# Kernel tuning notes

Measured on AMD Instinct MI355X. Metric: run time of the kernel, lower is better.

Reference implementation:

```python
import jax, jax.numpy as jnp
import numpy as np

B, N, H, A, S = 8, 8192, 256, 64, 32  # batch, nodes, hidden, annotation, sub_graphs


def _mysoftmax(x):
    # exp, zero out where x <= 0, normalize over last dim, nan (0/0) -> 0
    x_exp = jnp.where(x > 0, jnp.exp(x), 0.0)
    part = jnp.sum(x_exp, axis=-1, keepdims=True)
    # safe divide: where partition == 0 the faithful result after nan_to_num is 0
    return jnp.where(part > 0, x_exp / jnp.where(part > 0, part, 1.0), 0.0)


def setup_inputs() -> dict:
    key = jax.random.key(0)
    k1, k2, k3, k4, k5, k6 = jax.random.split(key, 6)
    x = jax.random.normal(k1, (B, N, H + A), dtype=jnp.float32)
    node_map = jax.random.uniform(k2, (B, S, N), dtype=jnp.float32)
    lim = 1.0 / np.sqrt(H + A)
    Wi = jax.random.uniform(k3, (H, H + A), minval=-lim, maxval=lim, dtype=jnp.float32)
    bi = jax.random.uniform(k4, (H,), minval=-lim, maxval=lim, dtype=jnp.float32)
    Wj = jax.random.uniform(k5, (H, H + A), minval=-lim, maxval=lim, dtype=jnp.float32)
    bj = jax.random.uniform(k6, (H,), minval=-lim, maxval=lim, dtype=jnp.float32)
    return {"x": x, "node_map": node_map, "Wi": Wi, "bi": bi, "Wj": Wj, "bj": bj}


def reference(x, node_map, Wi, bi, Wj, bj):
    # gated node features: sigmoid(fc_i(x)) * tanh(fc_j(x))  -> [B, N, H]
    x_sigm = jax.nn.sigmoid(jnp.einsum('bnf,hf->bnh', x, Wi) + bi)
    x_tanh = jnp.tanh(jnp.einsum('bnf,hf->bnh', x, Wj) + bj)
    x_all = x_sigm * x_tanh
    # per-node L2 norm -> [B, 1, N]
    x_norm = jnp.linalg.norm(x_all, axis=-1)[:, None, :]
    # scaled subgraph map and masked softmax over nodes -> [B, S, N]
    weight = _mysoftmax(node_map * x_norm)
    # weighted sum over nodes (replaces [B,S,N,H] broadcast) -> [B, S, H]
    pooled = jnp.einsum('bsn,bnh->bsh', weight, x_all)
    return jnp.tanh(pooled), weight[..., None]
```

## Files before the change

### kernel.cpp

```cpp
#include <hip/hip_runtime.h>
#include <cstdint>
#include <cstddef>

typedef unsigned short u16;
typedef unsigned int   u32;
using short8 = __attribute__((ext_vector_type(8))) short;
using f32x4  = __attribute__((ext_vector_type(4))) float;

#define NB    8
#define NN    8192
#define HH    256
#define FF    320
#define SS    32
#define NROWS 65536
#define NCH   64

__device__ __forceinline__ u16 f2bf(float f) {
    union { float f; u32 u; } v; v.f = f;
    u32 r = v.u + 0x7fffu + ((v.u >> 16) & 1u);
    return (u16)(r >> 16);
}
__device__ __forceinline__ u32 pk2h(float lo, float hi) {
    union { float f; u32 u; } a, b; a.f = lo; b.f = hi;
    return __builtin_amdgcn_perm(b.u + 0x8000u, a.u + 0x8000u, 0x07060302u);
}
__device__ __forceinline__ short8 pack8(float4 a, float4 b) {
    union { u32 u[4]; short8 s; } r;
    r.u[0] = pk2h(a.x, a.y); r.u[1] = pk2h(a.z, a.w);
    r.u[2] = pk2h(b.x, b.y); r.u[3] = pk2h(b.z, b.w);
    return r.s;
}

__global__ __launch_bounds__(256) void prep_w(const float* __restrict__ Wi,
                                              const float* __restrict__ Wj,
                                              u16* __restrict__ Wb) {
    int idx = blockIdx.x * 256 + threadIdx.x;
    float v = (idx < 81920) ? Wi[idx] : Wj[idx - 81920];
    Wb[idx] = f2bf(v);
}

__global__ __launch_bounds__(256) void cast_x(const float* __restrict__ x,
                                              u16* __restrict__ xb) {
    int t = blockIdx.x * 256 + threadIdx.x;
    #pragma unroll
    for (int i = 0; i < 4; ++i) {
        size_t g = (size_t)i * 655360 + t;
        float4 a = *reinterpret_cast<const float4*>(x + g * 8);
        float4 b = *reinterpret_cast<const float4*>(x + g * 8 + 4);
        *reinterpret_cast<short8*>(xb + g * 8) = pack8(a, b);
    }
}

__global__ __launch_bounds__(512, 4) void gemm_gate_pre(
    const u16* __restrict__ xbg, const u16* __restrict__ Wb,
    const float* __restrict__ bi, const float* __restrict__ bj,
    u16* __restrict__ xa, float* __restrict__ normsq_p)
{
    __shared__ u16 lB[5 * 8192];

    const int bx   = blockIdx.x;
    const int xcd  = bx & 7;
    const int ht   = (bx >> 3) & 3;
    const int slot = bx >> 5;
    const int mb   = xcd + slot * 8;
    const int m0   = mb * 256;
    const int h0   = ht * 64;
    const int b_idx = m0 >> 13;
    const int n0    = m0 & 8191;

    const int tid  = threadIdx.x;
    const int w    = tid >> 6;
    const int lane = tid & 63;
    const int quad = lane >> 4;
    const int l15  = lane & 15;

    {
        const int rsub = lane >> 3;
        const int kg   = (lane & 7) ^ rsub;
        #pragma unroll
        for (int kt = 0; kt < 5; ++kt) {
            #pragma unroll
            for (int j = 0; j < 2; ++j) {
                int sl  = w * 2 + j;
                int row = sl * 8 + rsub;
                int mat = row >> 6, hl = row & 63;
                const u16* gsrc = Wb + mat * 81920 + (size_t)(h0 + hl) * FF + kt * 64 + kg * 8;
                u16* ldst = &lB[kt * 8192 + sl * 512];
                __builtin_amdgcn_global_load_lds(
                    (const __attribute__((address_space(1))) void*)gsrc,
                    (__attribute__((address_space(3))) void*)ldst, 16, 0, 0);
            }
        }
    }

    const u16* xr0 = xbg + (size_t)(m0 + w * 32 + l15) * FF + quad * 8;
    const u16* xr1 = xr0 + 16 * FF;

    f32x4 acc[8][2];
    #pragma unroll
    for (int a = 0; a < 8; ++a)
        #pragma unroll
        for (int m = 0; m < 2; ++m) acc[a][m] = (f32x4){0.f, 0.f, 0.f, 0.f};

    short8 af[4][2];
    #pragma unroll
    for (int s = 0; s < 3; ++s) {
        af[s][0] = *reinterpret_cast<const short8*>(xr0 + s * 32);
        af[s][1] = *reinterpret_cast<const short8*>(xr1 + s * 32);
    }

    __syncthreads();

    #pragma unroll
    for (int ks = 0; ks < 10; ++ks) {
        const int kt  = ks >> 1, kk = ks & 1;
        const int cur = ks & 3;
        if (ks < 7) {
            const int nx = (ks + 3) & 3;
            af[nx][0] = *reinterpret_cast<const short8*>(xr0 + (ks + 3) * 32);
            af[nx][1] = *reinterpret_cast<const short8*>(xr1 + (ks + 3) * 32);
        }
        #pragma unroll
        for (int mn = 0; mn < 8; ++mn) {
            int c = mn * 16 + l15;
            short8 bv = *reinterpret_cast<const short8*>(
                &lB[kt * 8192 + c * 64 + (((kk * 4 + quad) ^ (c & 7)) << 3)]);
            acc[mn][0] = __builtin_amdgcn_mfma_f32_16x16x32_bf16(af[cur][0], bv, acc[mn][0], 0, 0, 0);
            acc[mn][1] = __builtin_amdgcn_mfma_f32_16x16x32_bf16(af[cur][1], bv, acc[mn][1], 0, 0, 0);
        }
    }

    float s0[2][4];
    #pragma unroll
    for (int mt = 0; mt < 2; ++mt)
        #pragma unroll
        for (int r = 0; r < 4; ++r) s0[mt][r] = 0.f;

    #pragma unroll
    for (int hq = 0; hq < 4; ++hq) {
        int h = h0 + hq * 16 + l15;
        float bi_v = bi[h], bj_v = bj[h];
        #pragma unroll
        for (int mt = 0; mt < 2; ++mt) {
            float xall[4];
            #pragma unroll
            for (int r = 0; r < 4; ++r) {
                float yi = acc[hq][mt][r] + bi_v;
                float yj = acc[hq + 4][mt][r] + bj_v;
                float sg = 1.f / (1.f + __expf(-yi));
                float e2 = __expf(-2.f * yj);
                float th = (1.f - e2) / (1.f + e2);
                float xv = sg * th;
                xall[r] = xv;
                s0[mt][r] += xv * xv;
            }
            uint2 pk;
            pk.x = pk2h(xall[0], xall[1]);
            pk.y = pk2h(xall[2], xall[3]);
            size_t o = (size_t)b_idx * ((size_t)HH * NN) + (size_t)h * NN
                     + (size_t)(n0 + w * 32 + mt * 16 + quad * 4);
            *reinterpret_cast<uint2*>(&xa[o]) = pk;
        }
    }
    #pragma unroll
    for (int m = 1; m <= 8; m <<= 1) {
        #pragma unroll
        for (int mt = 0; mt < 2; ++mt)
            #pragma unroll
            for (int r = 0; r < 4; ++r)
                s0[mt][r] += __shfl_xor(s0[mt][r], m, 64);
    }
    if (l15 == 0) {
        #pragma unroll
        for (int mt = 0; mt < 2; ++mt)
            #pragma unroll
            for (int r = 0; r < 4; ++r)
                normsq_p[ht * NROWS + m0 + w * 32 + mt * 16 + quad * 4 + r] = s0[mt][r];
    }
}

__global__ __launch_bounds__(512, 4) void gemm_gate_f32(
    const float* __restrict__ x, const u16* __restrict__ Wb,
    const float* __restrict__ bi, const float* __restrict__ bj,
    u16* __restrict__ xa, float* __restrict__ normsq_p)
{
    __shared__ u16 lB[5 * 8192];

    const int bx   = blockIdx.x;
    const int xcd  = bx & 7;
    const int ht   = (bx >> 3) & 3;
    const int slot = bx >> 5;
    const int mb   = xcd + slot * 8;
    const int m0   = mb * 256;
    const int h0   = ht * 64;
    const int b_idx = m0 >> 13;
    const int n0    = m0 & 8191;

    const int tid  = threadIdx.x;
    const int w    = tid >> 6;
    const int lane = tid & 63;
    const int quad = lane >> 4;
    const int l15  = lane & 15;

    {
        const int rsub = lane >> 3;
        const int kg   = (lane & 7) ^ rsub;
        #pragma unroll
        for (int kt = 0; kt < 5; ++kt) {
            #pragma unroll
            for (int j = 0; j < 2; ++j) {
                int sl  = w * 2 + j;
                int row = sl * 8 + rsub;
                int mat = row >> 6, hl = row & 63;
                const u16* gsrc = Wb + mat * 81920 + (size_t)(h0 + hl) * FF + kt * 64 + kg * 8;
                u16* ldst = &lB[kt * 8192 + sl * 512];
                __builtin_amdgcn_global_load_lds(
                    (const __attribute__((address_space(1))) void*)gsrc,
                    (__attribute__((address_space(3))) void*)ldst, 16, 0, 0);
            }
        }
    }

    const float* xb = x + (size_t)(m0 + w * 32 + l15) * FF + quad * 8;

    f32x4 acc[8][2];
    #pragma unroll
    for (int a = 0; a < 8; ++a)
        #pragma unroll
        for (int m = 0; m < 2; ++m) acc[a][m] = (f32x4){0.f, 0.f, 0.f, 0.f};

    float4 pre[3][2][2];
    #pragma unroll
    for (int s = 0; s < 2; ++s)
        #pragma unroll
        for (int mt = 0; mt < 2; ++mt) {
            pre[s][mt][0] = *reinterpret_cast<const float4*>(xb + mt * 16 * FF + s * 32);
            pre[s][mt][1] = *reinterpret_cast<const float4*>(xb + mt * 16 * FF + s * 32 + 4);
        }

    __syncthreads();

    #pragma unroll
    for (int ks = 0; ks < 10; ++ks) {
        const int kt  = ks >> 1, kk = ks & 1;
        const int cur = ks % 3;
        if (ks < 8) {
            const int nx = (ks + 2) % 3;
            const int f  = (ks + 2) * 32;
            #pragma unroll
            for (int mt = 0; mt < 2; ++mt) {
                pre[nx][mt][0] = *reinterpret_cast<const float4*>(xb + mt * 16 * FF + f);
                pre[nx][mt][1] = *reinterpret_cast<const float4*>(xb + mt * 16 * FF + f + 4);
            }
        }
        short8 af0 = pack8(pre[cur][0][0], pre[cur][0][1]);
        short8 af1 = pack8(pre[cur][1][0], pre[cur][1][1]);
        #pragma unroll
        for (int mn = 0; mn < 8; ++mn) {
            int c = mn * 16 + l15;
            short8 bv = *reinterpret_cast<const short8*>(
                &lB[kt * 8192 + c * 64 + (((kk * 4 + quad) ^ (c & 7)) << 3)]);
            acc[mn][0] = __builtin_amdgcn_mfma_f32_16x16x32_bf16(af0, bv, acc[mn][0], 0, 0, 0);
            acc[mn][1] = __builtin_amdgcn_mfma_f32_16x16x32_bf16(af1, bv, acc[mn][1], 0, 0, 0);
        }
    }

    float s0[2][4];
    #pragma unroll
    for (int mt = 0; mt < 2; ++mt)
        #pragma unroll
        for (int r = 0; r < 4; ++r) s0[mt][r] = 0.f;

    #pragma unroll
    for (int hq = 0; hq < 4; ++hq) {
        int h = h0 + hq * 16 + l15;
        float bi_v = bi[h], bj_v = bj[h];
        #pragma unroll
        for (int mt = 0; mt < 2; ++mt) {
            float xall[4];
            #pragma unroll
            for (int r = 0; r < 4; ++r) {
                float yi = acc[hq][mt][r] + bi_v;
                float yj = acc[hq + 4][mt][r] + bj_v;
                float sg = 1.f / (1.f + __expf(-yi));
                float e2 = __expf(-2.f * yj);
                float th = (1.f - e2) / (1.f + e2);
                float xv = sg * th;
                xall[r] = xv;
                s0[mt][r] += xv * xv;
            }
            uint2 pk;
            pk.x = pk2h(xall[0], xall[1]);
            pk.y = pk2h(xall[2], xall[3]);
            size_t o = (size_t)b_idx * ((size_t)HH * NN) + (size_t)h * NN
                     + (size_t)(n0 + w * 32 + mt * 16 + quad * 4);
            *reinterpret_cast<uint2*>(&xa[o]) = pk;
        }
    }
    #pragma unroll
    for (int m = 1; m <= 8; m <<= 1) {
        #pragma unroll
        for (int mt = 0; mt < 2; ++mt)
            #pragma unroll
            for (int r = 0; r < 4; ++r)
                s0[mt][r] += __shfl_xor(s0[mt][r], m, 64);
    }
    if (l15 == 0) {
        #pragma unroll
        for (int mt = 0; mt < 2; ++mt)
            #pragma unroll
            for (int r = 0; r < 4; ++r)
                normsq_p[ht * NROWS + m0 + w * 32 + mt * 16 + quad * 4 + r] = s0[mt][r];
    }
}

__global__ __launch_bounds__(1024) void softmax_k(
    const float* __restrict__ nm, const float* __restrict__ normsq_p,
    float* __restrict__ out1)
{
    __shared__ float red[16];
    int bs = blockIdx.x;
    int b  = bs >> 5;
    const float* src = nm + (size_t)bs * NN;
    float* dst       = out1 + (size_t)bs * NN;
    const float* ns  = normsq_p + (size_t)b * NN;
    int tid = threadIdx.x;
    float e[8];
    float sum = 0.f;
    #pragma unroll
    for (int i = 0; i < 8; ++i) {
        int n = i * 1024 + tid;
        float nsq = ns[n] + ns[n + NROWS] + ns[n + 2 * NROWS] + ns[n + 3 * NROWS];
        float logit = src[n] * sqrtf(nsq);
        float v = (logit > 0.f) ? __expf(logit) : 0.f;
        e[i] = v;
        sum += v;
    }
    #pragma unroll
    for (int m = 1; m <= 32; m <<= 1) sum += __shfl_xor(sum, m, 64);
    int w = tid >> 6, lane = tid & 63;
    if (lane == 0) red[w] = sum;
    __syncthreads();
    float part = 0.f;
    #pragma unroll
    for (int j = 0; j < 16; ++j) part += red[j];
    float inv = (part > 0.f) ? (1.f / part) : 0.f;
    #pragma unroll
    for (int i = 0; i < 8; ++i) dst[i * 1024 + tid] = e[i] * inv;
}

__global__ __launch_bounds__(256) void pooled_k(
    const u16* __restrict__ xa, const float* __restrict__ wgt,
    float* __restrict__ part)
{
    __shared__ u16 lw[32 * 136];
    int bx = blockIdx.x;
    int b  = bx >> 6, c = bx & 63;
    int n0 = c * 128;
    int tid = threadIdx.x, w = tid >> 6, lane = tid & 63, quad = lane >> 4, l15 = lane & 15;

    const u16* ab = xa + (size_t)b * ((size_t)HH * NN) + n0;

    short8 av[2][4];
    #pragma unroll
    for (int htl = 0; htl < 4; ++htl) {
        int h = w * 64 + htl * 16 + l15;
        av[0][htl] = *reinterpret_cast<const short8*>(ab + (size_t)h * NN + quad * 8);
    }

    {
        int s  = tid >> 3;
        int jq = (tid & 7) * 16;
        const float* src = wgt + (size_t)(b * SS + s) * NN + n0 + jq;
        #pragma unroll
        for (int q = 0; q < 4; ++q) {
            float4 v = *reinterpret_cast<const float4*>(src + q * 4);
            uint2 pk;
            pk.x = pk2h(v.x, v.y);
            pk.y = pk2h(v.z, v.w);
            *reinterpret_cast<uint2*>(&lw[s * 136 + jq + q * 4]) = pk;
        }
    }
    __syncthreads();

    f32x4 acc[4][2];
    #pragma unroll
    for (int a = 0; a < 4; ++a)
        #pragma unroll
        for (int s = 0; s < 2; ++s) acc[a][s] = (f32x4){0.f, 0.f, 0.f, 0.f};

    #pragma unroll
    for (int ks = 0; ks < 4; ++ks) {
        const int cur = ks & 1, nxt = cur ^ 1;
        if (ks < 3) {
            #pragma unroll
            for (int htl = 0; htl < 4; ++htl) {
                int h = w * 64 + htl * 16 + l15;
                av[nxt][htl] = *reinterpret_cast<const short8*>(
                    ab + (size_t)h * NN + (ks + 1) * 32 + quad * 8);
            }
        }
        #pragma unroll
        for (int st = 0; st < 2; ++st) {
            int s = st * 16 + l15;
            short8 bv = *reinterpret_cast<const short8*>(&lw[s * 136 + ks * 32 + quad * 8]);
            #pragma unroll
            for (int htl = 0; htl < 4; ++htl)
                acc[htl][st] = __builtin_amdgcn_mfma_f32_16x16x32_bf16(av[cur][htl], bv, acc[htl][st], 0, 0, 0);
        }
    }
    float* pb = part + (size_t)(b * NCH + c) * 8192;
    #pragma unroll
    for (int htl = 0; htl < 4; ++htl) {
        #pragma unroll
        for (int st = 0; st < 2; ++st) {
            int h = w * 64 + htl * 16 + quad * 4;
            int s = st * 16 + l15;
            *reinterpret_cast<f32x4*>(&pb[s * 256 + h]) = acc[htl][st];
        }
    }
}

__global__ __launch_bounds__(256) void reduce_tanh(const float* __restrict__ part,
                                                   float* __restrict__ out0)
{
    int gid = blockIdx.x * 256 + threadIdx.x;
    int b = gid >> 13, r = gid & 8191;
    const float* p = part + (size_t)b * NCH * 8192 + r;
    float s = 0.f;
    #pragma unroll
    for (int c = 0; c < NCH; ++c) s += p[(size_t)c * 8192];
    out0[gid] = tanhf(s);
}

extern "C" void kernel_launch(void* const* d_in, const int* in_sizes, int n_in,
                              void* d_out, int out_size, void* d_ws, size_t ws_size,
                              hipStream_t stream) {
    const float* x  = (const float*)d_in[0];
    const float* nm = (const float*)d_in[1];
    const float* Wi = (const float*)d_in[2];
    const float* bi = (const float*)d_in[3];
    const float* Wj = (const float*)d_in[4];
    const float* bj = (const float*)d_in[5];
    float* out0 = (float*)d_out;
    float* out1 = out0 + NB * SS * HH;

    char* ws = (char*)d_ws;
    size_t off = 0;
    u16*   Wb       = (u16*)(ws + off);  off += 327680;
    u16*   xa       = (u16*)(ws + off);  off += 33554432;
    float* normsq_p = (float*)(ws + off); off += 1048576;
    float* part     = (float*)(ws + off); off += 16777216;
    u16*   xb       = (u16*)(ws + off);
    const size_t need_fast = off + 41943040;

    prep_w<<<640, 256, 0, stream>>>(Wi, Wj, Wb);
    if (ws_size >= need_fast) {
        cast_x       <<<2560, 256, 0, stream>>>(x, xb);
        gemm_gate_pre<<<1024, 512, 0, stream>>>(xb, Wb, bi, bj, xa, normsq_p);
    } else {
        gemm_gate_f32<<<1024, 512, 0, stream>>>(x, Wb, bi, bj, xa, normsq_p);
    }
    softmax_k  <<<256, 1024, 0, stream>>>(nm, normsq_p, out1);
    pooled_k   <<<512,  256, 0, stream>>>(xa, out1, part);
    reduce_tanh<<<256,  256, 0, stream>>>(part, out0);
}
```

Measured before the change: 215.0 us.

## Retile gate GEMM warps to 2x2, merge prep kernels, halve pooled chunks

The gate GEMM now splits its eight waves into a 4x2 grid, each covering 64 rows by 32 columns of both the i and j outputs. This replaces 32 rows by all 64 columns and is meant to raise A-fragment reuse and cut global A loads per wave. The norm partials grow from four to eight slices, so softmax now sums eight. The weight and x cast kernels are merged into one launch. Pooling uses 256-node chunks, halving the partial buffer and the reduction work, at the cost of fewer blocks and more accumulator registers per wave.

Result: no change. 211.7 us (-1.5%).

```diff
diff --git a/kernel.cpp b/kernel.cpp
--- a/kernel.cpp
+++ b/kernel.cpp
@@ -13,7 +13,7 @@
 #define FF    320
 #define SS    32
 #define NROWS 65536
-#define NCH   64
+#define NCH   32
 
 __device__ __forceinline__ u16 f2bf(float f) {
     union { float f; u32 u; } v; v.f = f;
@@ -31,23 +31,25 @@
     return r.s;
 }
 
-__global__ __launch_bounds__(256) void prep_w(const float* __restrict__ Wi,
-                                              const float* __restrict__ Wj,
-                                              u16* __restrict__ Wb) {
-    int idx = blockIdx.x * 256 + threadIdx.x;
-    float v = (idx < 81920) ? Wi[idx] : Wj[idx - 81920];
-    Wb[idx] = f2bf(v);
-}
-
-__global__ __launch_bounds__(256) void cast_x(const float* __restrict__ x,
-                                              u16* __restrict__ xb) {
-    int t = blockIdx.x * 256 + threadIdx.x;
-    #pragma unroll
-    for (int i = 0; i < 4; ++i) {
-        size_t g = (size_t)i * 655360 + t;
-        float4 a = *reinterpret_cast<const float4*>(x + g * 8);
-        float4 b = *reinterpret_cast<const float4*>(x + g * 8 + 4);
-        *reinterpret_cast<short8*>(xb + g * 8) = pack8(a, b);
+__global__ __launch_bounds__(256) void prep_all(const float* __restrict__ Wi,
+                                                const float* __restrict__ Wj,
+                                                const float* __restrict__ x,
+                                                u16* __restrict__ Wb,
+                                                u16* __restrict__ xb) {
+    int bx = blockIdx.x;
+    if (bx < 640) {
+        int idx = bx * 256 + threadIdx.x;
+        float v = (idx < 81920) ? Wi[idx] : Wj[idx - 81920];
+        Wb[idx] = f2bf(v);
+    } else {
+        int t = (bx - 640) * 256 + threadIdx.x;
+        #pragma unroll
+        for (int i = 0; i < 4; ++i) {
+            size_t g = (size_t)i * 655360 + t;
+            float4 a = *reinterpret_cast<const float4*>(x + g * 8);
+            float4 b = *reinterpret_cast<const float4*>(x + g * 8 + 4);
+            *reinterpret_cast<short8*>(xb + g * 8) = pack8(a, b);
+        }
     }
 }
 
@@ -73,6 +75,8 @@
     const int lane = tid & 63;
     const int quad = lane >> 4;
     const int l15  = lane & 15;
+    const int rg   = w >> 1;
+    const int cg   = w & 1;
 
     {
         const int rsub = lane >> 3;
@@ -93,60 +97,61 @@
         }
     }
 
-    const u16* xr0 = xbg + (size_t)(m0 + w * 32 + l15) * FF + quad * 8;
-    const u16* xr1 = xr0 + 16 * FF;
-
-    f32x4 acc[8][2];
-    #pragma unroll
-    for (int a = 0; a < 8; ++a)
-        #pragma unroll
-        for (int m = 0; m < 2; ++m) acc[a][m] = (f32x4){0.f, 0.f, 0.f, 0.f};
-
-    short8 af[4][2];
-    #pragma unroll
-    for (int s = 0; s < 3; ++s) {
-        af[s][0] = *reinterpret_cast<const short8*>(xr0 + s * 32);
-        af[s][1] = *reinterpret_cast<const short8*>(xr1 + s * 32);
-    }
+    const u16* xr = xbg + (size_t)(m0 + rg * 64 + l15) * FF + quad * 8;
+
+    f32x4 acc[4][4];
+    #pragma unroll
+    for (int a = 0; a < 4; ++a)
+        #pragma unroll
+        for (int m = 0; m < 4; ++m) acc[a][m] = (f32x4){0.f, 0.f, 0.f, 0.f};
+
+    short8 af[2][4];
+    #pragma unroll
+    for (int mt = 0; mt < 4; ++mt)
+        af[0][mt] = *reinterpret_cast<const short8*>(xr + mt * 16 * FF);
+
+    const int cb0 = cg * 32, cb1 = cg * 32 + 16, cb2 = 64 + cg * 32, cb3 = 64 + cg * 32 + 16;
 
     __syncthreads();
 
     #pragma unroll
     for (int ks = 0; ks < 10; ++ks) {
         const int kt  = ks >> 1, kk = ks & 1;
-        const int cur = ks & 3;
-        if (ks < 7) {
-            const int nx = (ks + 3) & 3;
-            af[nx][0] = *reinterpret_cast<const short8*>(xr0 + (ks + 3) * 32);
-            af[nx][1] = *reinterpret_cast<const short8*>(xr1 + (ks + 3) * 32);
-        }
-        #pragma unroll
-        for (int mn = 0; mn < 8; ++mn) {
-            int c = mn * 16 + l15;
+        const int cur = ks & 1, nxt = cur ^ 1;
+        if (ks < 9) {
+            #pragma unroll
+            for (int mt = 0; mt < 4; ++mt)
+                af[nxt][mt] = *reinterpret_cast<const short8*>(xr + mt * 16 * FF + (ks + 1) * 32);
+        }
+        const int cbs[4] = {cb0, cb1, cb2, cb3};
+        #pragma unroll
+        for (int mn = 0; mn < 4; ++mn) {
+            int c = cbs[mn] + l15;
             short8 bv = *reinterpret_cast<const short8*>(
                 &lB[kt * 8192 + c * 64 + (((kk * 4 + quad) ^ (c & 7)) << 3)]);
-            acc[mn][0] = __builtin_amdgcn_mfma_f32_16x16x32_bf16(af[cur][0], bv, acc[mn][0], 0, 0, 0);
-            acc[mn][1] = __builtin_amdgcn_mfma_f32_16x16x32_bf16(af[cur][1], bv, acc[mn][1], 0, 0, 0);
-        }
-    }
-
-    float s0[2][4];
-    #pragma unroll
-    for (int mt = 0; mt < 2; ++mt)
+            #pragma unroll
+            for (int mt = 0; mt < 4; ++mt)
+                acc[mn][mt] = __builtin_amdgcn_mfma_f32_16x16x32_bf16(af[cur][mt], bv, acc[mn][mt], 0, 0, 0);
+        }
+    }
+
+    float s0[4][4];
+    #pragma unroll
+    for (int mt = 0; mt < 4; ++mt)
         #pragma unroll
         for (int r = 0; r < 4; ++r) s0[mt][r] = 0.f;
 
     #pragma unroll
-    for (int hq = 0; hq < 4; ++hq) {
-        int h = h0 + hq * 16 + l15;
+    for (int hq = 0; hq < 2; ++hq) {
+        int h = h0 + cg * 32 + hq * 16 + l15;
         float bi_v = bi[h], bj_v = bj[h];
         #pragma unroll
-        for (int mt = 0; mt < 2; ++mt) {
+        for (int mt = 0; mt < 4; ++mt) {
             float xall[4];
             #pragma unroll
             for (int r = 0; r < 4; ++r) {
                 float yi = acc[hq][mt][r] + bi_v;
-                float yj = acc[hq + 4][mt][r] + bj_v;
+                float yj = acc[hq + 2][mt][r] + bj_v;
                 float sg = 1.f / (1.f + __expf(-yi));
                 float e2 = __expf(-2.f * yj);
                 float th = (1.f - e2) / (1.f + e2);
@@ -158,24 +163,24 @@
             pk.x = pk2h(xall[0], xall[1]);
             pk.y = pk2h(xall[2], xall[3]);
             size_t o = (size_t)b_idx * ((size_t)HH * NN) + (size_t)h * NN
-                     + (size_t)(n0 + w * 32 + mt * 16 + quad * 4);
+                     + (size_t)(n0 + rg * 64 + mt * 16 + quad * 4);
             *reinterpret_cast<uint2*>(&xa[o]) = pk;
         }
     }
     #pragma unroll
     for (int m = 1; m <= 8; m <<= 1) {
         #pragma unroll
-        for (int mt = 0; mt < 2; ++mt)
+        for (int mt = 0; mt < 4; ++mt)
             #pragma unroll
             for (int r = 0; r < 4; ++r)
                 s0[mt][r] += __shfl_xor(s0[mt][r], m, 64);
     }
     if (l15 == 0) {
         #pragma unroll
-        for (int mt = 0; mt < 2; ++mt)
+        for (int mt = 0; mt < 4; ++mt)
             #pragma unroll
             for (int r = 0; r < 4; ++r)
-                normsq_p[ht * NROWS + m0 + w * 32 + mt * 16 + quad * 4 + r] = s0[mt][r];
+                normsq_p[(ht * 2 + cg) * NROWS + m0 + rg * 64 + mt * 16 + quad * 4 + r] = s0[mt][r];
     }
 }
 
@@ -330,7 +335,9 @@
     #pragma unroll
     for (int i = 0; i < 8; ++i) {
         int n = i * 1024 + tid;
-        float nsq = ns[n] + ns[n + NROWS] + ns[n + 2 * NROWS] + ns[n + 3 * NROWS];
+        float nsq = 0.f;
+        #pragma unroll
+        for (int j = 0; j < 8; ++j) nsq += ns[n + j * NROWS];
         float logit = src[n] * sqrtf(nsq);
         float v = (logit > 0.f) ? __expf(logit) : 0.f;
         e[i] = v;
@@ -353,10 +360,10 @@
     const u16* __restrict__ xa, const float* __restrict__ wgt,
     float* __restrict__ part)
 {
-    __shared__ u16 lw[32 * 136];
+    __shared__ u16 lw[32 * 264];
     int bx = blockIdx.x;
-    int b  = bx >> 6, c = bx & 63;
-    int n0 = c * 128;
+    int b  = bx >> 5, c = bx & 31;
+    int n0 = c * 256;
     int tid = threadIdx.x, w = tid >> 6, lane = tid & 63, quad = lane >> 4, l15 = lane & 15;
 
     const u16* ab = xa + (size_t)b * ((size_t)HH * NN) + n0;
@@ -370,15 +377,15 @@
 
     {
         int s  = tid >> 3;
-        int jq = (tid & 7) * 16;
-        const float* src = wgt + (size_t)(b * SS + s) * NN + n0 + jq;
-        #pragma unroll
-        for (int q = 0; q < 4; ++q) {
+        int nb = (tid & 7) * 32;
+        const float* src = wgt + (size_t)(b * SS + s) * NN + n0 + nb;
+        #pragma unroll
+        for (int q = 0; q < 8; ++q) {
             float4 v = *reinterpret_cast<const float4*>(src + q * 4);
             uint2 pk;
             pk.x = pk2h(v.x, v.y);
             pk.y = pk2h(v.z, v.w);
-            *reinterpret_cast<uint2*>(&lw[s * 136 + jq + q * 4]) = pk;
+            *reinterpret_cast<uint2*>(&lw[s * 264 + nb + q * 4]) = pk;
         }
     }
     __syncthreads();
@@ -390,9 +397,9 @@
         for (int s = 0; s < 2; ++s) acc[a][s] = (f32x4){0.f, 0.f, 0.f, 0.f};
 
     #pragma unroll
-    for (int ks = 0; ks < 4; ++ks) {
+    for (int ks = 0; ks < 8; ++ks) {
         const int cur = ks & 1, nxt = cur ^ 1;
-        if (ks < 3) {
+        if (ks < 7) {
             #pragma unroll
             for (int htl = 0; htl < 4; ++htl) {
                 int h = w * 64 + htl * 16 + l15;
@@ -403,7 +410,7 @@
         #pragma unroll
         for (int st = 0; st < 2; ++st) {
             int s = st * 16 + l15;
-            short8 bv = *reinterpret_cast<const short8*>(&lw[s * 136 + ks * 32 + quad * 8]);
+            short8 bv = *reinterpret_cast<const short8*>(&lw[s * 264 + ks * 32 + quad * 8]);
             #pragma unroll
             for (int htl = 0; htl < 4; ++htl)
                 acc[htl][st] = __builtin_amdgcn_mfma_f32_16x16x32_bf16(av[cur][htl], bv, acc[htl][st], 0, 0, 0);
@@ -447,21 +454,22 @@
 
     char* ws = (char*)d_ws;
     size_t off = 0;
-    u16*   Wb       = (u16*)(ws + off);  off += 327680;
-    u16*   xa       = (u16*)(ws + off);  off += 33554432;
-    float* normsq_p = (float*)(ws + off); off += 1048576;
-    float* part     = (float*)(ws + off); off += 16777216;
+    u16*   Wb       = (u16*)(ws + off);   off += 327680;
+    u16*   xa       = (u16*)(ws + off);   off += 33554432;
+    float* normsq_p = (float*)(ws + off); off += 2097152;
+    float* part     = (float*)(ws + off); off += 8388608;
     u16*   xb       = (u16*)(ws + off);
     const size_t need_fast = off + 41943040;
 
-    prep_w<<<640, 256, 0, stream>>>(Wi, Wj, Wb);
     if (ws_size >= need_fast) {
-        cast_x       <<<2560, 256, 0, stream>>>(x, xb);
+        prep_all     <<<3200, 256, 0, stream>>>(Wi, Wj, x, Wb, xb);
         gemm_gate_pre<<<1024, 512, 0, stream>>>(xb, Wb, bi, bj, xa, normsq_p);
     } else {
+        prep_all     <<<640,  256, 0, stream>>>(Wi, Wj, x, Wb, xb);
+        hipMemsetAsync(normsq_p + 4 * NROWS, 0, 4 * NROWS * sizeof(float), stream);
         gemm_gate_f32<<<1024, 512, 0, stream>>>(x, Wb, bi, bj, xa, normsq_p);
     }
     softmax_k  <<<256, 1024, 0, stream>>>(nm, normsq_p, out1);
-    pooled_k   <<<512,  256, 0, stream>>>(xa, out1, part);
+    pooled_k   <<<256,  256, 0, stream>>>(xa, out1, part);
     reduce_tanh<<<256,  256, 0, stream>>>(part, out0);
 }
```

## Merge prep kernels, reuse staged weights across two row tiles, widen pooled chunks

Applied to the files above, without the earlier changes.

Folds the weight cast and the x cast into one launch. Each gate GEMM block now processes two 256-row tiles, so the LDS-staged weight slice is loaded once for both and half as many blocks are launched. The pooled kernel covers 256 nodes per block instead of 128, which halves the partial-sum buffer and the work left for the reduce step. The cost is fewer blocks in flight on the GPU, with less parallelism to hide latency in the GEMM and pooled kernels.

Measured after the change: 206.6 us. -3.9%, faster.

```diff
diff --git a/kernel.cpp b/kernel.cpp
--- a/kernel.cpp
+++ b/kernel.cpp
@@ -13,7 +13,7 @@
 #define FF    320
 #define SS    32
 #define NROWS 65536
-#define NCH   64
+#define NCH   32
 
 __device__ __forceinline__ u16 f2bf(float f) {
     union { float f; u32 u; } v; v.f = f;
@@ -31,23 +31,25 @@
     return r.s;
 }
 
-__global__ __launch_bounds__(256) void prep_w(const float* __restrict__ Wi,
-                                              const float* __restrict__ Wj,
-                                              u16* __restrict__ Wb) {
-    int idx = blockIdx.x * 256 + threadIdx.x;
-    float v = (idx < 81920) ? Wi[idx] : Wj[idx - 81920];
-    Wb[idx] = f2bf(v);
-}
-
-__global__ __launch_bounds__(256) void cast_x(const float* __restrict__ x,
-                                              u16* __restrict__ xb) {
-    int t = blockIdx.x * 256 + threadIdx.x;
-    #pragma unroll
-    for (int i = 0; i < 4; ++i) {
-        size_t g = (size_t)i * 655360 + t;
-        float4 a = *reinterpret_cast<const float4*>(x + g * 8);
-        float4 b = *reinterpret_cast<const float4*>(x + g * 8 + 4);
-        *reinterpret_cast<short8*>(xb + g * 8) = pack8(a, b);
+__global__ __launch_bounds__(256) void prep_all(const float* __restrict__ Wi,
+                                                const float* __restrict__ Wj,
+                                                const float* __restrict__ x,
+                                                u16* __restrict__ Wb,
+                                                u16* __restrict__ xb) {
+    int bx = blockIdx.x;
+    if (bx < 640) {
+        int idx = bx * 256 + threadIdx.x;
+        float v = (idx < 81920) ? Wi[idx] : Wj[idx - 81920];
+        Wb[idx] = f2bf(v);
+    } else {
+        int t = (bx - 640) * 256 + threadIdx.x;
+        #pragma unroll
+        for (int i = 0; i < 4; ++i) {
+            size_t g = (size_t)i * 655360 + t;
+            float4 a = *reinterpret_cast<const float4*>(x + g * 8);
+            float4 b = *reinterpret_cast<const float4*>(x + g * 8 + 4);
+            *reinterpret_cast<short8*>(xb + g * 8) = pack8(a, b);
+        }
     }
 }
 
@@ -62,11 +64,7 @@
     const int xcd  = bx & 7;
     const int ht   = (bx >> 3) & 3;
     const int slot = bx >> 5;
-    const int mb   = xcd + slot * 8;
-    const int m0   = mb * 256;
     const int h0   = ht * 64;
-    const int b_idx = m0 >> 13;
-    const int n0    = m0 & 8191;
 
     const int tid  = threadIdx.x;
     const int w    = tid >> 6;
@@ -93,89 +91,98 @@
         }
     }
 
-    const u16* xr0 = xbg + (size_t)(m0 + w * 32 + l15) * FF + quad * 8;
-    const u16* xr1 = xr0 + 16 * FF;
-
-    f32x4 acc[8][2];
-    #pragma unroll
-    for (int a = 0; a < 8; ++a)
-        #pragma unroll
-        for (int m = 0; m < 2; ++m) acc[a][m] = (f32x4){0.f, 0.f, 0.f, 0.f};
-
+    f32x4  acc[8][2];
     short8 af[4][2];
-    #pragma unroll
-    for (int s = 0; s < 3; ++s) {
-        af[s][0] = *reinterpret_cast<const short8*>(xr0 + s * 32);
-        af[s][1] = *reinterpret_cast<const short8*>(xr1 + s * 32);
-    }
-
-    __syncthreads();
-
-    #pragma unroll
-    for (int ks = 0; ks < 10; ++ks) {
-        const int kt  = ks >> 1, kk = ks & 1;
-        const int cur = ks & 3;
-        if (ks < 7) {
-            const int nx = (ks + 3) & 3;
-            af[nx][0] = *reinterpret_cast<const short8*>(xr0 + (ks + 3) * 32);
-            af[nx][1] = *reinterpret_cast<const short8*>(xr1 + (ks + 3) * 32);
-        }
-        #pragma unroll
-        for (int mn = 0; mn < 8; ++mn) {
-            int c = mn * 16 + l15;
-            short8 bv = *reinterpret_cast<const short8*>(
-                &lB[kt * 8192 + c * 64 + (((kk * 4 + quad) ^ (c & 7)) << 3)]);
-            acc[mn][0] = __builtin_amdgcn_mfma_f32_16x16x32_bf16(af[cur][0], bv, acc[mn][0], 0, 0, 0);
-            acc[mn][1] = __builtin_amdgcn_mfma_f32_16x16x32_bf16(af[cur][1], bv, acc[mn][1], 0, 0, 0);
-        }
-    }
-
-    float s0[2][4];
-    #pragma unroll
-    for (int mt = 0; mt < 2; ++mt)
-        #pragma unroll
-        for (int r = 0; r < 4; ++r) s0[mt][r] = 0.f;
-
-    #pragma unroll
-    for (int hq = 0; hq < 4; ++hq) {
-        int h = h0 + hq * 16 + l15;
-        float bi_v = bi[h], bj_v = bj[h];
-        #pragma unroll
-        for (int mt = 0; mt < 2; ++mt) {
-            float xall[4];
-            #pragma unroll
-            for (int r = 0; r < 4; ++r) {
-                float yi = acc[hq][mt][r] + bi_v;
-                float yj = acc[hq + 4][mt][r] + bj_v;
-                float sg = 1.f / (1.f + __expf(-yi));
-                float e2 = __expf(-2.f * yj);
-                float th = (1.f - e2) / (1.f + e2);
-                float xv = sg * th;
-                xall[r] = xv;
-                s0[mt][r] += xv * xv;
-            }
-            uint2 pk;
-            pk.x = pk2h(xall[0], xall[1]);
-            pk.y = pk2h(xall[2], xall[3]);
-            size_t o = (size_t)b_idx * ((size_t)HH * NN) + (size_t)h * NN
-                     + (size_t)(n0 + w * 32 + mt * 16 + quad * 4);
-            *reinterpret_cast<uint2*>(&xa[o]) = pk;
-        }
-    }
-    #pragma unroll
-    for (int m = 1; m <= 8; m <<= 1) {
+
+    #pragma unroll
+    for (int mi = 0; mi < 2; ++mi) {
+        const int mb    = xcd + (slot * 2 + mi) * 8;
+        const int m0    = mb * 256;
+        const int b_idx = m0 >> 13;
+        const int n0    = m0 & 8191;
+
+        const u16* xr0 = xbg + (size_t)(m0 + w * 32 + l15) * FF + quad * 8;
+        const u16* xr1 = xr0 + 16 * FF;
+
+        #pragma unroll
+        for (int a = 0; a < 8; ++a)
+            #pragma unroll
+            for (int m = 0; m < 2; ++m) acc[a][m] = (f32x4){0.f, 0.f, 0.f, 0.f};
+
+        #pragma unroll
+        for (int s = 0; s < 3; ++s) {
+            af[s][0] = *reinterpret_cast<const short8*>(xr0 + s * 32);
+            af[s][1] = *reinterpret_cast<const short8*>(xr1 + s * 32);
+        }
+
+        if (mi == 0) __syncthreads();
+
+        #pragma unroll
+        for (int ks = 0; ks < 10; ++ks) {
+            const int kt  = ks >> 1, kk = ks & 1;
+            const int cur = ks & 3;
+            if (ks < 7) {
+                const int nx = (ks + 3) & 3;
+                af[nx][0] = *reinterpret_cast<const short8*>(xr0 + (ks + 3) * 32);
+                af[nx][1] = *reinterpret_cast<const short8*>(xr1 + (ks + 3) * 32);
+            }
+            #pragma unroll
+            for (int mn = 0; mn < 8; ++mn) {
+                int c = mn * 16 + l15;
+                short8 bv = *reinterpret_cast<const short8*>(
+                    &lB[kt * 8192 + c * 64 + (((kk * 4 + quad) ^ (c & 7)) << 3)]);
+                acc[mn][0] = __builtin_amdgcn_mfma_f32_16x16x32_bf16(af[cur][0], bv, acc[mn][0], 0, 0, 0);
+                acc[mn][1] = __builtin_amdgcn_mfma_f32_16x16x32_bf16(af[cur][1], bv, acc[mn][1], 0, 0, 0);
+            }
+        }
+
+        float s0[2][4];
         #pragma unroll
         for (int mt = 0; mt < 2; ++mt)
             #pragma unroll
-            for (int r = 0; r < 4; ++r)
-                s0[mt][r] += __shfl_xor(s0[mt][r], m, 64);
-    }
-    if (l15 == 0) {
-        #pragma unroll
-        for (int mt = 0; mt < 2; ++mt)
-            #pragma unroll
-            for (int r = 0; r < 4; ++r)
-                normsq_p[ht * NROWS + m0 + w * 32 + mt * 16 + quad * 4 + r] = s0[mt][r];
+            for (int r = 0; r < 4; ++r) s0[mt][r] = 0.f;
+
+        #pragma unroll
+        for (int hq = 0; hq < 4; ++hq) {
+            int h = h0 + hq * 16 + l15;
+            float bi_v = bi[h], bj_v = bj[h];
+            #pragma unroll
+            for (int mt = 0; mt < 2; ++mt) {
+                float xall[4];
+                #pragma unroll
+                for (int r = 0; r < 4; ++r) {
+                    float yi = acc[hq][mt][r] + bi_v;
+                    float yj = acc[hq + 4][mt][r] + bj_v;
+                    float sg = 1.f / (1.f + __expf(-yi));
+                    float e2 = __expf(-2.f * yj);
+                    float th = (1.f - e2) / (1.f + e2);
+                    float xv = sg * th;
+                    xall[r] = xv;
+                    s0[mt][r] += xv * xv;
+                }
+                uint2 pk;
+                pk.x = pk2h(xall[0], xall[1]);
+                pk.y = pk2h(xall[2], xall[3]);
+                size_t o = (size_t)b_idx * ((size_t)HH * NN) + (size_t)h * NN
+                         + (size_t)(n0 + w * 32 + mt * 16 + quad * 4);
+                *reinterpret_cast<uint2*>(&xa[o]) = pk;
+            }
+        }
+        #pragma unroll
+        for (int m = 1; m <= 8; m <<= 1) {
+            #pragma unroll
+            for (int mt = 0; mt < 2; ++mt)
+                #pragma unroll
+                for (int r = 0; r < 4; ++r)
+                    s0[mt][r] += __shfl_xor(s0[mt][r], m, 64);
+        }
+        if (l15 == 0) {
+            #pragma unroll
+            for (int mt = 0; mt < 2; ++mt)
+                #pragma unroll
+                for (int r = 0; r < 4; ++r)
+                    normsq_p[ht * NROWS + m0 + w * 32 + mt * 16 + quad * 4 + r] = s0[mt][r];
+        }
     }
 }
 
@@ -353,10 +360,10 @@
     const u16* __restrict__ xa, const float* __restrict__ wgt,
     float* __restrict__ part)
 {
-    __shared__ u16 lw[32 * 136];
+    __shared__ u16 lw[32 * 264];
     int bx = blockIdx.x;
-    int b  = bx >> 6, c = bx & 63;
-    int n0 = c * 128;
+    int b  = bx >> 5, c = bx & 31;
+    int n0 = c * 256;
     int tid = threadIdx.x, w = tid >> 6, lane = tid & 63, quad = lane >> 4, l15 = lane & 15;
 
     const u16* ab = xa + (size_t)b * ((size_t)HH * NN) + n0;
@@ -370,15 +377,15 @@
 
     {
         int s  = tid >> 3;
-        int jq = (tid & 7) * 16;
-        const float* src = wgt + (size_t)(b * SS + s) * NN + n0 + jq;
-        #pragma unroll
-        for (int q = 0; q < 4; ++q) {
+        int nb = (tid & 7) * 32;
+        const float* src = wgt + (size_t)(b * SS + s) * NN + n0 + nb;
+        #pragma unroll
+        for (int q = 0; q < 8; ++q) {
             float4 v = *reinterpret_cast<const float4*>(src + q * 4);
             uint2 pk;
             pk.x = pk2h(v.x, v.y);
             pk.y = pk2h(v.z, v.w);
-            *reinterpret_cast<uint2*>(&lw[s * 136 + jq + q * 4]) = pk;
+            *reinterpret_cast<uint2*>(&lw[s * 264 + nb + q * 4]) = pk;
         }
     }
     __syncthreads();
@@ -390,9 +397,9 @@
         for (int s = 0; s < 2; ++s) acc[a][s] = (f32x4){0.f, 0.f, 0.f, 0.f};
 
     #pragma unroll
-    for (int ks = 0; ks < 4; ++ks) {
+    for (int ks = 0; ks < 8; ++ks) {
         const int cur = ks & 1, nxt = cur ^ 1;
-        if (ks < 3) {
+        if (ks < 7) {
             #pragma unroll
             for (int htl = 0; htl < 4; ++htl) {
                 int h = w * 64 + htl * 16 + l15;
@@ -403,7 +410,7 @@
         #pragma unroll
         for (int st = 0; st < 2; ++st) {
             int s = st * 16 + l15;
-            short8 bv = *reinterpret_cast<const short8*>(&lw[s * 136 + ks * 32 + quad * 8]);
+            short8 bv = *reinterpret_cast<const short8*>(&lw[s * 264 + ks * 32 + quad * 8]);
             #pragma unroll
             for (int htl = 0; htl < 4; ++htl)
                 acc[htl][st] = __builtin_amdgcn_mfma_f32_16x16x32_bf16(av[cur][htl], bv, acc[htl][st], 0, 0, 0);
@@ -447,21 +454,21 @@
 
     char* ws = (char*)d_ws;
     size_t off = 0;
-    u16*   Wb       = (u16*)(ws + off);  off += 327680;
-    u16*   xa       = (u16*)(ws + off);  off += 33554432;
+    u16*   Wb       = (u16*)(ws + off);   off += 327680;
+    u16*   xa       = (u16*)(ws + off);   off += 33554432;
     float* normsq_p = (float*)(ws + off); off += 1048576;
-    float* part     = (float*)(ws + off); off += 16777216;
+    float* part     = (float*)(ws + off); off += 8388608;
     u16*   xb       = (u16*)(ws + off);
     const size_t need_fast = off + 41943040;
 
-    prep_w<<<640, 256, 0, stream>>>(Wi, Wj, Wb);
     if (ws_size >= need_fast) {
-        cast_x       <<<2560, 256, 0, stream>>>(x, xb);
-        gemm_gate_pre<<<1024, 512, 0, stream>>>(xb, Wb, bi, bj, xa, normsq_p);
+        prep_all     <<<3200, 256, 0, stream>>>(Wi, Wj, x, Wb, xb);
+        gemm_gate_pre<<<512,  512, 0, stream>>>(xb, Wb, bi, bj, xa, normsq_p);
     } else {
+        prep_all     <<<640,  256, 0, stream>>>(Wi, Wj, x, Wb, xb);
         gemm_gate_f32<<<1024, 512, 0, stream>>>(x, Wb, bi, bj, xa, normsq_p);
     }
     softmax_k  <<<256, 1024, 0, stream>>>(nm, normsq_p, out1);
-    pooled_k   <<<512,  256, 0, stream>>>(xa, out1, part);
+    pooled_k   <<<256,  256, 0, stream>>>(xa, out1, part);
     reduce_tanh<<<256,  256, 0, stream>>>(part, out0);
 }
```
